# Kernel tuning notes

Hardware: AMD Instinct MI355X
Metric: run time of the kernel (lower is better)

The kernel has to match this reference:

```python
import jax, jax.numpy as jnp
import numpy as np

N_NODES = 100
F_IN = 65536
C_OUT = 60
ACTION_DIM = 100
N_EDGES = 2000


def setup_inputs() -> dict:
    key = jax.random.key(0)
    ks = jax.random.split(key, 16)
    s = 0.02
    return {
        "substrate_features": jax.random.normal(ks[0], (1, N_NODES, F_IN), jnp.float32),
        "edge_index": jax.random.randint(ks[1], (2, N_EDGES), 0, N_NODES, dtype=jnp.int32),
        "v_cpu_demand_t": jax.random.uniform(ks[2], (1,), jnp.float32),
        "v_bw_demand_t": jax.random.uniform(ks[3], (1,), jnp.float32),
        "num_pending_v_nodes_t": jax.random.uniform(ks[4], (1,), jnp.float32),
        "actor_w": jax.random.normal(ks[5], (3, F_IN, C_OUT), jnp.float32) * s,
        "actor_b": jax.random.normal(ks[6], (C_OUT,), jnp.float32) * s,
        "critic_w": jax.random.normal(ks[7], (3, F_IN, C_OUT), jnp.float32) * s,
        "critic_b": jax.random.normal(ks[8], (C_OUT,), jnp.float32) * s,
        "actor_fc_w": jax.random.normal(ks[9], (N_NODES * C_OUT + 3, ACTION_DIM), jnp.float32) * s,
        "actor_fc_b": jax.random.normal(ks[10], (ACTION_DIM,), jnp.float32) * s,
        "critic_fc_w": jax.random.normal(ks[11], (N_NODES * C_OUT + 3, 1), jnp.float32) * s,
        "critic_fc_b": jax.random.normal(ks[12], (1,), jnp.float32) * s,
    }


def cheb_conv(x, edge_index, W, b):
    # ChebConv, K=3, sym normalization, lambda_max=2 (PyG defaults).
    # With lambda_max=2 the scaled Laplacian is L_hat = -D^{-1/2} A D^{-1/2}
    # (diagonal becomes 0 after the -1 self-loop shift).
    # x: [1, N, F]; edge_index: [2, E]; W: [3, F, C]; b: [C]
    src, dst = edge_index[0], edge_index[1]
    n = x.shape[1]
    deg = jax.ops.segment_sum(jnp.ones(src.shape[0], x.dtype), src, num_segments=n)
    dis = jnp.where(deg > 0, jax.lax.rsqrt(jnp.where(deg > 0, deg, 1.0)), 0.0)
    norm = -(dis[src] * dis[dst])  # [E], L_hat off-diagonal entries
    x2 = x[0]  # [N, F]

    def prop(z):  # z: [N, F] -> L_hat @ z via gather/scatter over edges
        return jax.ops.segment_sum(z[src] * norm[:, None], dst, num_segments=n)

    Tx0 = x2
    Tx1 = prop(Tx0)
    Tx2 = 2.0 * prop(Tx1) - Tx0
    out = Tx0 @ W[0] + Tx1 @ W[1] + Tx2 @ W[2] + b  # [N, C]
    return out[None]  # [1, N, C]


def reference(substrate_features, edge_index, v_cpu_demand_t, v_bw_demand_t,
              num_pending_v_nodes_t, actor_w, actor_b, critic_w, critic_b,
              actor_fc_w, actor_fc_b, critic_fc_w, critic_fc_b):
    emb_a = jnp.tanh(cheb_conv(substrate_features, edge_index, actor_w, actor_b))
    emb_a = emb_a.reshape(1, -1)  # [1, N*60]
    emb_c = jnp.tanh(cheb_conv(substrate_features, edge_index, critic_w, critic_b))
    emb_c = emb_c.reshape(1, -1)
    extras = [v_cpu_demand_t[None], v_bw_demand_t[None], num_pending_v_nodes_t[None]]  # each [1,1]
    state_a = jnp.concatenate([emb_a] + extras, axis=1)  # [1, 6003]
    state_c = jnp.concatenate([emb_c] + extras, axis=1)
    logits = state_a @ actor_fc_w + actor_fc_b  # [1, action_dim]
    values = state_c @ critic_fc_w + critic_fc_b  # [1, 1]
    return (logits, values)
```

## Files before the change

kernel.cpp:

```cpp
#include <hip/hip_runtime.h>
#include <stdint.h>

#define F_IN 65536
#define NN 100
#define CO 60
#define KC 512
#define BK 64
#define NIT (KC/BK)
#define NSPLIT (F_IN/KC)
#define AST 72

typedef short v8s __attribute__((ext_vector_type(8)));
typedef float v4f __attribute__((ext_vector_type(4)));

__device__ __forceinline__ unsigned short f2bf(float x){
  unsigned int u = __float_as_uint(x);
  u += 0x7fffu + ((u>>16)&1u);
  return (unsigned short)(u>>16);
}

__global__ __launch_bounds__(256,2)
void k_gemm(const float* __restrict__ x, const float* __restrict__ aw,
            const float* __restrict__ cw, float* __restrict__ Y){
  const int ksplit = blockIdx.x;
  const int gk = blockIdx.y;
  const int k0 = ksplit*KC;
  const int tid = threadIdx.x;
  const int wave = tid>>6, lane = tid&63, quad = lane>>4, nl = lane&15;
  const int c0 = wave*16;
  const int ccl = min(c0+nl, CO-1);

  __shared__ __align__(16) unsigned short Al[112*AST];

  const float* ap = aw + (size_t)gk*F_IN*CO + (size_t)(k0 + quad*8)*CO + ccl;
  const float* cp = cw + (size_t)gk*F_IN*CO + (size_t)(k0 + quad*8)*CO + ccl;

  v4f accA[7], accC[7];
  #pragma unroll
  for(int i=0;i<7;i++){
    v4f z = {0.f,0.f,0.f,0.f};
    accA[i]=z; accC[i]=z;
  }

  for(int it=0; it<NIT; ++it){
    const int kb = k0 + it*BK;
    float bA[16], bC[16];
    #pragma unroll
    for(int u=0; u<16; ++u){
      const int koff = (it*BK + (u>>3)*32 + (u&7))*CO;
      bA[u] = ap[koff];
      bC[u] = cp[koff];
    }
    #pragma unroll
    for(int p=0;p<7;++p){
      int lin = p*256 + tid;
      int row = lin>>4, q = lin&15;
      int rcl = min(row, NN-1);
      const float4 v = *(const float4*)(x + (size_t)rcl*F_IN + kb + q*4);
      uint2 w;
      w.x = (unsigned)f2bf(v.x) | ((unsigned)f2bf(v.y)<<16);
      w.y = (unsigned)f2bf(v.z) | ((unsigned)f2bf(v.w)<<16);
      ((uint2*)Al)[row*18 + q];
      ((uint2*)Al)[row*18 + q] = w;
    }
    __syncthreads();
    v8s fA0,fA1,fC0,fC1;
    #pragma unroll
    for(int j=0;j<8;++j){
      fA0[j]=(short)f2bf(bA[j]);   fA1[j]=(short)f2bf(bA[8+j]);
      fC0[j]=(short)f2bf(bC[j]);   fC1[j]=(short)f2bf(bC[8+j]);
    }
    #pragma unroll
    for(int mt=0; mt<7; ++mt){
      const unsigned short* arow = Al + (mt*16+nl)*AST + quad*8;
      v8s a0 = *(const v8s*)(arow);
      v8s a1 = *(const v8s*)(arow+32);
      accA[mt] = __builtin_amdgcn_mfma_f32_16x16x32_bf16(a0,fA0,accA[mt],0,0,0);
      accA[mt] = __builtin_amdgcn_mfma_f32_16x16x32_bf16(a1,fA1,accA[mt],0,0,0);
      accC[mt] = __builtin_amdgcn_mfma_f32_16x16x32_bf16(a0,fC0,accC[mt],0,0,0);
      accC[mt] = __builtin_amdgcn_mfma_f32_16x16x32_bf16(a1,fC1,accC[mt],0,0,0);
    }
    __syncthreads();
  }
  const int c = c0 + nl;
  if (c < CO){
    #pragma unroll
    for(int mt=0; mt<7; ++mt){
      #pragma unroll
      for(int i=0;i<4;++i){
        int m = mt*16 + quad*4 + i;
        if (m < NN){
          atomicAdd(&Y[(size_t)gk*NN*CO     + m*CO + c], accA[mt][i]);
          atomicAdd(&Y[(size_t)(3+gk)*NN*CO + m*CO + c], accC[mt][i]);
        }
      }
    }
  }
}

__global__ void k_cheb(const float* __restrict__ Y, const int* __restrict__ ei,
                       const float* __restrict__ ab, const float* __restrict__ cb,
                       float* __restrict__ emb){
  const int net = blockIdx.x / CO;
  const int c   = blockIdx.x % CO;
  const int t   = threadIdx.x;
  __shared__ float L[NN][NN+1];
  __shared__ float dis[NN];
  __shared__ int   deg[NN];
  __shared__ float y0[NN], y1[NN], y2[NN], zu[NN];

  for(int i=t;i<NN*(NN+1);i+=128) ((float*)L)[i]=0.f;
  if(t<NN) deg[t]=0;
  __syncthreads();
  for(int e=t;e<2000;e+=128) atomicAdd(&deg[ei[e]],1);
  __syncthreads();
  if(t<NN) dis[t] = deg[t]>0 ? rsqrtf((float)deg[t]) : 0.f;
  __syncthreads();
  for(int e=t;e<2000;e+=128){
    int s = ei[e], d = ei[2000+e];
    atomicAdd(&L[d][s], -dis[s]*dis[d]);
  }
  if(t<NN){
    const float* yb = Y + (size_t)net*3*NN*CO + t*CO + c;
    y0[t]=yb[0]; y1[t]=yb[NN*CO]; y2[t]=yb[2*NN*CO];
  }
  __syncthreads();
  if(t<NN){
    float s=0.f;
    #pragma unroll 4
    for(int j=0;j<NN;++j) s += L[t][j]*y2[j];
    zu[t] = y1[t] + 2.f*s;
  }
  __syncthreads();
  if(t<NN){
    float s=0.f;
    #pragma unroll 4
    for(int j=0;j<NN;++j) s += L[t][j]*zu[j];
    float b = (net==0) ? ab[c] : cb[c];
    emb[net*NN*CO + t*CO + c] = tanhf(y0[t] - y2[t] + s + b);
  }
}

__global__ void k_fc(const float* __restrict__ emb, const float* __restrict__ afw,
                     const float* __restrict__ afb, const float* __restrict__ cfw,
                     const float* __restrict__ cfb, const float* __restrict__ s0,
                     const float* __restrict__ s1, const float* __restrict__ s2,
                     float* __restrict__ out){
  const int j = blockIdx.x;
  const int t = threadIdx.x;
  float p = 0.f;
  if(j < 100){
    for(int i=t;i<6000;i+=256) p += emb[i]*afw[(size_t)i*100 + j];
  } else {
    const float* e = emb + 6000;
    for(int i=t;i<6000;i+=256) p += e[i]*cfw[i];
  }
  #pragma unroll
  for(int o=32;o>0;o>>=1) p += __shfl_down(p,o,64);
  __shared__ float red[4];
  if((t&63)==0) red[t>>6]=p;
  __syncthreads();
  if(t==0){
    float tot = red[0]+red[1]+red[2]+red[3];
    if(j<100){
      tot += s0[0]*afw[6000*100+j] + s1[0]*afw[6001*100+j] + s2[0]*afw[6002*100+j] + afb[j];
    } else {
      tot += s0[0]*cfw[6000] + s1[0]*cfw[6001] + s2[0]*cfw[6002] + cfb[0];
    }
    out[j] = tot;
  }
}

extern "C" void kernel_launch(void* const* d_in, const int* in_sizes, int n_in,
                              void* d_out, int out_size, void* d_ws, size_t ws_size,
                              hipStream_t stream){
  const float* x   = (const float*)d_in[0];
  const int*   ei  = (const int*)d_in[1];
  const float* s0  = (const float*)d_in[2];
  const float* s1  = (const float*)d_in[3];
  const float* s2  = (const float*)d_in[4];
  const float* aw  = (const float*)d_in[5];
  const float* ab  = (const float*)d_in[6];
  const float* cw  = (const float*)d_in[7];
  const float* cb  = (const float*)d_in[8];
  const float* afw = (const float*)d_in[9];
  const float* afb = (const float*)d_in[10];
  const float* cfw = (const float*)d_in[11];
  const float* cfb = (const float*)d_in[12];
  float* out = (float*)d_out;

  float* Y   = (float*)d_ws;
  float* emb = Y + 6*NN*CO;

  hipMemsetAsync(Y, 0, 6*NN*CO*sizeof(float), stream);
  k_gemm<<<dim3(NSPLIT,3), 256, 0, stream>>>(x, aw, cw, Y);
  k_cheb<<<120, 128, 0, stream>>>(Y, ei, ab, cb, emb);
  k_fc<<<101, 256, 0, stream>>>(emb, afw, afb, cfw, cfb, s0, s1, s2, out);
}
```

Baseline: 254.9 us.

## Double-buffer GEMM tiles, split actor/critic blocks, add partial-sum reduction, rework FC

The GEMM now runs one weight set per block on a 128x6 grid instead of computing actor and critic in the same block on a 128x3 grid. It double-buffers the LDS A tile and prefetches the next x and weight chunk into registers, which also removes one barrier per iteration. When workspace allows, per-split partial results go to a buffer and a separate reduce kernel sums them, replacing heavy atomic contention on Y. The FC kernel is restructured so 25 blocks cover column strips with coalesced weight reads and atomics into the zeroed output. The costs are an extra kernel launch, an extra memset and more partial-buffer traffic, and the x tile is now converted twice because actor and critic blocks no longer share it.

```diff
diff --git a/kernel.cpp b/kernel.cpp
--- a/kernel.cpp
+++ b/kernel.cpp
@@ -4,98 +4,134 @@
 #define F_IN 65536
 #define NN 100
 #define CO 60
-#define KC 512
+#define G_SPLIT 128
+#define KC (F_IN/G_SPLIT)
 #define BK 64
 #define NIT (KC/BK)
-#define NSPLIT (F_IN/KC)
 #define AST 72
 
 typedef short v8s __attribute__((ext_vector_type(8)));
 typedef float v4f __attribute__((ext_vector_type(4)));
 
-__device__ __forceinline__ unsigned short f2bf(float x){
+__device__ __forceinline__ unsigned int f2bf(float x){
   unsigned int u = __float_as_uint(x);
   u += 0x7fffu + ((u>>16)&1u);
-  return (unsigned short)(u>>16);
+  return u>>16;
+}
+
+__device__ __forceinline__ v4f mfma16(v8s a, v8s b, v4f c){
+  return __builtin_amdgcn_mfma_f32_16x16x32_bf16(a,b,c,0,0,0);
 }
 
 __global__ __launch_bounds__(256,2)
 void k_gemm(const float* __restrict__ x, const float* __restrict__ aw,
-            const float* __restrict__ cw, float* __restrict__ Y){
-  const int ksplit = blockIdx.x;
-  const int gk = blockIdx.y;
-  const int k0 = ksplit*KC;
+            const float* __restrict__ cw, float* __restrict__ dst, int partial){
+  const int s  = blockIdx.x;
+  const int g  = blockIdx.y;
+  const int k0 = s*KC;
   const int tid = threadIdx.x;
   const int wave = tid>>6, lane = tid&63, quad = lane>>4, nl = lane&15;
   const int c0 = wave*16;
   const int ccl = min(c0+nl, CO-1);
 
-  __shared__ __align__(16) unsigned short Al[112*AST];
-
-  const float* ap = aw + (size_t)gk*F_IN*CO + (size_t)(k0 + quad*8)*CO + ccl;
-  const float* cp = cw + (size_t)gk*F_IN*CO + (size_t)(k0 + quad*8)*CO + ccl;
-
-  v4f accA[7], accC[7];
+  const float* W  = (g<3) ? (aw + (size_t)g*F_IN*CO) : (cw + (size_t)(g-3)*F_IN*CO);
+  const float* wp = W + (size_t)(k0 + quad*8)*CO + ccl;
+
+  __shared__ __align__(16) unsigned short Al[2][112*AST];
+
+  float4 ra[7];
+  float  rb[16];
   #pragma unroll
-  for(int i=0;i<7;i++){
-    v4f z = {0.f,0.f,0.f,0.f};
-    accA[i]=z; accC[i]=z;
-  }
+  for(int p=0;p<7;++p){
+    int lin = p*256 + tid, row = lin>>4, q = lin&15;
+    int rcl = min(row, NN-1);
+    ra[p] = *(const float4*)(x + (size_t)rcl*F_IN + k0 + q*4);
+  }
+  #pragma unroll
+  for(int u=0;u<16;++u) rb[u] = wp[((u>>3)*32 + (u&7))*CO];
+
+  v4f acc[7];
+  #pragma unroll
+  for(int i=0;i<7;++i){ v4f z={0.f,0.f,0.f,0.f}; acc[i]=z; }
 
   for(int it=0; it<NIT; ++it){
-    const int kb = k0 + it*BK;
-    float bA[16], bC[16];
-    #pragma unroll
-    for(int u=0; u<16; ++u){
-      const int koff = (it*BK + (u>>3)*32 + (u&7))*CO;
-      bA[u] = ap[koff];
-      bC[u] = cp[koff];
-    }
+    unsigned short* buf = Al[it&1];
     #pragma unroll
     for(int p=0;p<7;++p){
-      int lin = p*256 + tid;
-      int row = lin>>4, q = lin&15;
-      int rcl = min(row, NN-1);
-      const float4 v = *(const float4*)(x + (size_t)rcl*F_IN + kb + q*4);
+      int lin = p*256 + tid, row = lin>>4, q = lin&15;
       uint2 w;
-      w.x = (unsigned)f2bf(v.x) | ((unsigned)f2bf(v.y)<<16);
-      w.y = (unsigned)f2bf(v.z) | ((unsigned)f2bf(v.w)<<16);
-      ((uint2*)Al)[row*18 + q];
-      ((uint2*)Al)[row*18 + q] = w;
+      w.x = f2bf(ra[p].x) | (f2bf(ra[p].y)<<16);
+      w.y = f2bf(ra[p].z) | (f2bf(ra[p].w)<<16);
+      *(uint2*)(buf + row*AST + q*4) = w;
+    }
+    v8s fB0, fB1;
+    #pragma unroll
+    for(int j=0;j<8;++j){
+      fB0[j] = (short)f2bf(rb[j]);
+      fB1[j] = (short)f2bf(rb[8+j]);
     }
     __syncthreads();
-    v8s fA0,fA1,fC0,fC1;
-    #pragma unroll
-    for(int j=0;j<8;++j){
-      fA0[j]=(short)f2bf(bA[j]);   fA1[j]=(short)f2bf(bA[8+j]);
-      fC0[j]=(short)f2bf(bC[j]);   fC1[j]=(short)f2bf(bC[8+j]);
+    if(it+1 < NIT){
+      const int kb = k0 + (it+1)*BK;
+      #pragma unroll
+      for(int p=0;p<7;++p){
+        int lin = p*256 + tid, row = lin>>4, q = lin&15;
+        int rcl = min(row, NN-1);
+        ra[p] = *(const float4*)(x + (size_t)rcl*F_IN + kb + q*4);
+      }
+      #pragma unroll
+      for(int u=0;u<16;++u) rb[u] = wp[((it+1)*BK + (u>>3)*32 + (u&7))*CO];
     }
     #pragma unroll
     for(int mt=0; mt<7; ++mt){
-      const unsigned short* arow = Al + (mt*16+nl)*AST + quad*8;
+      const unsigned short* arow = buf + (mt*16+nl)*AST + quad*8;
       v8s a0 = *(const v8s*)(arow);
       v8s a1 = *(const v8s*)(arow+32);
-      accA[mt] = __builtin_amdgcn_mfma_f32_16x16x32_bf16(a0,fA0,accA[mt],0,0,0);
-      accA[mt] = __builtin_amdgcn_mfma_f32_16x16x32_bf16(a1,fA1,accA[mt],0,0,0);
-      accC[mt] = __builtin_amdgcn_mfma_f32_16x16x32_bf16(a0,fC0,accC[mt],0,0,0);
-      accC[mt] = __builtin_amdgcn_mfma_f32_16x16x32_bf16(a1,fC1,accC[mt],0,0,0);
-    }
-    __syncthreads();
-  }
+      acc[mt] = mfma16(a0, fB0, acc[mt]);
+      acc[mt] = mfma16(a1, fB1, acc[mt]);
+    }
+  }
+
   const int c = c0 + nl;
-  if (c < CO){
-    #pragma unroll
-    for(int mt=0; mt<7; ++mt){
-      #pragma unroll
-      for(int i=0;i<4;++i){
-        int m = mt*16 + quad*4 + i;
-        if (m < NN){
-          atomicAdd(&Y[(size_t)gk*NN*CO     + m*CO + c], accA[mt][i]);
-          atomicAdd(&Y[(size_t)(3+gk)*NN*CO + m*CO + c], accC[mt][i]);
+  if(c < CO){
+    if(partial){
+      float* pd = dst + ((size_t)g*G_SPLIT + s)*(NN*CO);
+      #pragma unroll
+      for(int mt=0;mt<7;++mt){
+        #pragma unroll
+        for(int i=0;i<4;++i){
+          int m = mt*16 + quad*4 + i;
+          if(m < NN) pd[m*CO + c] = acc[mt][i];
         }
       }
-    }
-  }
+    } else {
+      float* pd = dst + (size_t)g*(NN*CO);
+      #pragma unroll
+      for(int mt=0;mt<7;++mt){
+        #pragma unroll
+        for(int i=0;i<4;++i){
+          int m = mt*16 + quad*4 + i;
+          if(m < NN) atomicAdd(pd + m*CO + c, acc[mt][i]);
+        }
+      }
+    }
+  }
+}
+
+__global__ void k_reduce(const float* __restrict__ P, float* __restrict__ Y){
+  int o = blockIdx.x*256 + threadIdx.x;
+  if(o >= 6*NN*CO) return;
+  int gg = o/(NN*CO), r = o - gg*(NN*CO);
+  const float* p = P + (size_t)gg*G_SPLIT*(NN*CO) + (size_t)blockIdx.y*32*(NN*CO) + r;
+  float a0=0.f,a1=0.f,a2=0.f,a3=0.f;
+  #pragma unroll 2
+  for(int s4=0;s4<32;s4+=4){
+    a0 += p[(s4  )*(NN*CO)];
+    a1 += p[(s4+1)*(NN*CO)];
+    a2 += p[(s4+2)*(NN*CO)];
+    a3 += p[(s4+3)*(NN*CO)];
+  }
+  atomicAdd(&Y[o], (a0+a1)+(a2+a3));
 }
 
 __global__ void k_cheb(const float* __restrict__ Y, const int* __restrict__ ei,
@@ -141,33 +177,41 @@
   }
 }
 
+#define FCB 25
 __global__ void k_fc(const float* __restrict__ emb, const float* __restrict__ afw,
                      const float* __restrict__ afb, const float* __restrict__ cfw,
                      const float* __restrict__ cfb, const float* __restrict__ s0,
                      const float* __restrict__ s1, const float* __restrict__ s2,
                      float* __restrict__ out){
-  const int j = blockIdx.x;
+  const int b = blockIdx.x;
   const int t = threadIdx.x;
-  float p = 0.f;
-  if(j < 100){
-    for(int i=t;i<6000;i+=256) p += emb[i]*afw[(size_t)i*100 + j];
+  if(b < FCB){
+    const int jj = t & 127, half = t >> 7;
+    if(jj < 100){
+      const int i0 = b*240 + half*120;
+      const float* w = afw + (size_t)i0*100 + jj;
+      const float* e = emb + i0;
+      float p = 0.f;
+      #pragma unroll 4
+      for(int i=0;i<120;++i) p += e[i]*w[(size_t)i*100];
+      atomicAdd(&out[jj], p);
+    }
   } else {
+    float p = 0.f;
     const float* e = emb + 6000;
     for(int i=t;i<6000;i+=256) p += e[i]*cfw[i];
-  }
-  #pragma unroll
-  for(int o=32;o>0;o>>=1) p += __shfl_down(p,o,64);
-  __shared__ float red[4];
-  if((t&63)==0) red[t>>6]=p;
-  __syncthreads();
-  if(t==0){
-    float tot = red[0]+red[1]+red[2]+red[3];
-    if(j<100){
-      tot += s0[0]*afw[6000*100+j] + s1[0]*afw[6001*100+j] + s2[0]*afw[6002*100+j] + afb[j];
-    } else {
-      tot += s0[0]*cfw[6000] + s1[0]*cfw[6001] + s2[0]*cfw[6002] + cfb[0];
-    }
-    out[j] = tot;
+    #pragma unroll
+    for(int o=32;o>0;o>>=1) p += __shfl_down(p,o,64);
+    __shared__ float red[4];
+    if((t&63)==0) red[t>>6]=p;
+    __syncthreads();
+    if(t==0){
+      float tot = red[0]+red[1]+red[2]+red[3];
+      out[100] = tot + s0[0]*cfw[6000] + s1[0]*cfw[6001] + s2[0]*cfw[6002] + cfb[0];
+    }
+    if(t<100){
+      atomicAdd(&out[t], afb[t] + s0[0]*afw[600000+t] + s1[0]*afw[600100+t] + s2[0]*afw[600200+t]);
+    }
   }
 }
 
@@ -191,9 +235,17 @@
 
   float* Y   = (float*)d_ws;
   float* emb = Y + 6*NN*CO;
+  float* P   = emb + 2*NN*CO;
+  const size_t need = (size_t)(6*NN*CO + 2*NN*CO + (size_t)6*G_SPLIT*NN*CO)*sizeof(float);
+  const int partial = (ws_size >= need) ? 1 : 0;
 
   hipMemsetAsync(Y, 0, 6*NN*CO*sizeof(float), stream);
-  k_gemm<<<dim3(NSPLIT,3), 256, 0, stream>>>(x, aw, cw, Y);
+  hipMemsetAsync(out, 0, 101*sizeof(float), stream);
+
+  k_gemm<<<dim3(G_SPLIT,6), 256, 0, stream>>>(x, aw, cw, partial ? P : Y, partial);
+  if(partial){
+    k_reduce<<<dim3((6*NN*CO+255)/256, 4), 256, 0, stream>>>(P, Y);
+  }
   k_cheb<<<120, 128, 0, stream>>>(Y, ei, ab, cb, emb);
-  k_fc<<<101, 256, 0, stream>>>(emb, afw, afb, cfw, cfb, s0, s1, s2, out);
-}
+  k_fc<<<FCB+1, 256, 0, stream>>>(emb, afw, afb, cfw, cfb, s0, s1, s2, out);
+}
```

Result: faster. 212.4 us (-16.6%).
